# Kernel optimization log

Measured on AMD Instinct MI355X. Metric: run time of the kernel, lower is better.

The kernel has to match this reference:

```python
import jax, jax.numpy as jnp
import numpy as np

B, T, E = 2, 2048, 1024
H = 16
DH = E // H  # 64
DFF = 4 * E
EPS = 1e-5


def _layernorm(x, gamma, beta):
    mu = jnp.mean(x, axis=-1, keepdims=True)
    var = jnp.mean((x - mu) ** 2, axis=-1, keepdims=True)
    return (x - mu) * jax.lax.rsqrt(var + EPS) * gamma + beta


def setup_inputs() -> dict:
    key = jax.random.key(0)
    ks = jax.random.split(key, 16)
    s_e = 1.0 / np.sqrt(E)
    s_f = 1.0 / np.sqrt(DFF)
    return {
        "x": jax.random.normal(ks[0], (B, T, E), jnp.float32),
        # per-head QKV projections, stacked over heads [H, E, DH]
        "Wq": jax.random.normal(ks[1], (H, E, DH), jnp.float32) * s_e,
        "bq": jnp.zeros((H, DH), jnp.float32),
        "Wk": jax.random.normal(ks[2], (H, E, DH), jnp.float32) * s_e,
        "bk": jnp.zeros((H, DH), jnp.float32),
        "Wv": jax.random.normal(ks[3], (H, E, DH), jnp.float32) * s_e,
        "bv": jnp.zeros((H, DH), jnp.float32),
        # output projection
        "Wo": jax.random.normal(ks[4], (E, E), jnp.float32) * s_e,
        "bo": jnp.zeros((E,), jnp.float32),
        # feed-forward
        "W1": jax.random.normal(ks[5], (E, DFF), jnp.float32) * s_e,
        "b1": jnp.zeros((DFF,), jnp.float32),
        "W2": jax.random.normal(ks[6], (DFF, E), jnp.float32) * s_f,
        "b2": jnp.zeros((E,), jnp.float32),
        # layernorms
        "gamma1": jnp.ones((E,), jnp.float32),
        "beta1": jnp.zeros((E,), jnp.float32),
        "gamma2": jnp.ones((E,), jnp.float32),
        "beta2": jnp.zeros((E,), jnp.float32),
    }


def reference(x, Wq, bq, Wk, bk, Wv, bv, Wo, bo, W1, b1, W2, b2,
              gamma1, beta1, gamma2, beta2):
    Bc, Tc, Ec = x.shape
    # --- multi-head causal self-attention (dropout = eval/identity) ---
    xn = _layernorm(x, gamma1, beta1)
    q = jnp.einsum('bte,hed->bhtd', xn, Wq) + bq[:, None, :]
    k = jnp.einsum('bte,hed->bhtd', xn, Wk) + bk[:, None, :]
    v = jnp.einsum('bte,hed->bhtd', xn, Wv) + bv[:, None, :]
    scale = 1.0 / np.sqrt(q.shape[-1])
    scores = jnp.einsum('bhtd,bhsd->bhts', q, k) * scale  # [B,H,T,T]
    causal = jnp.tril(jnp.ones((Tc, Tc), bool))
    scores = jnp.where(causal, scores, jnp.float32(-1e9))
    attn = jax.nn.softmax(scores, axis=-1)
    out = jnp.einsum('bhts,bhsd->bhtd', attn, v)          # [B,H,T,DH]
    out = out.transpose(0, 2, 1, 3).reshape(Bc, Tc, Ec)    # concat heads
    out = out @ Wo + bo
    x = x + out
    # --- feed-forward ---
    xn2 = _layernorm(x, gamma2, beta2)
    h = jax.nn.relu(xn2 @ W1 + b1)
    x = x + (h @ W2 + b2)
    return x
```

## Files before the change

### kernel.cpp

```cpp
#include <hip/hip_runtime.h>
#include <stdint.h>

#define BT    4096
#define EDIM  1024
#define TLEN  2048
#define NH    16
#define DHH   64
#define DFFN  4096

typedef short short8 __attribute__((ext_vector_type(8)));
typedef float f32x4  __attribute__((ext_vector_type(4)));

typedef const __attribute__((address_space(1))) unsigned int* gas_ptr;
typedef __attribute__((address_space(3))) unsigned int*       las_ptr;

__device__ __forceinline__ float bf2f(unsigned short u) {
    union { unsigned int i; float f; } c; c.i = ((unsigned int)u) << 16; return c.f;
}
__device__ __forceinline__ unsigned short f2bf(float f) {
    union { float f; unsigned int i; } c; c.f = f;
    unsigned int u = c.i;
    unsigned int r = u + 0x7fffu + ((u >> 16) & 1u);
    return (unsigned short)(r >> 16);
}
__device__ __forceinline__ unsigned short f2bf_trunc(float f) {
    union { float f; unsigned int i; } c; c.f = f;
    return (unsigned short)(c.i >> 16);
}
__device__ __forceinline__ float fexp2(float x) {
#if __has_builtin(__builtin_amdgcn_exp2f)
    return __builtin_amdgcn_exp2f(x);
#else
    return __expf(x * 0.69314718056f);
#endif
}
__device__ __forceinline__ void gload16(const unsigned short* g, unsigned short* l) {
    __builtin_amdgcn_global_load_lds((gas_ptr)g, (las_ptr)l, 16, 0, 0);
}

#define CS_SCALE 0.18033688011f

template<int QKV>
__global__ __launch_bounds__(256) void transpose_kernel(
    const float* src, unsigned short* dst, int Kdim, int srcStride)
{
    __shared__ float T[64][65];
    int t = threadIdx.x;
    int n0 = blockIdx.x * 64, k0 = blockIdx.y * 64;
    int r = t >> 4, c4 = (t & 15) * 4;
    #pragma unroll
    for (int i = 0; i < 4; i++) {
        int rr = r + i * 16;
        const float* p;
        if (QKV) p = src + ((size_t)(n0 >> 6)) * 65536 + (size_t)(k0 + rr) * 64 + c4;
        else     p = src + (size_t)(k0 + rr) * srcStride + n0 + c4;
        float4 v = *(const float4*)p;
        T[c4 + 0][rr] = v.x;
        T[c4 + 1][rr] = v.y;
        T[c4 + 2][rr] = v.z;
        T[c4 + 3][rr] = v.w;
    }
    __syncthreads();
    int rn = t >> 2, ck = (t & 3) * 16;
    short8 o0, o1;
    #pragma unroll
    for (int j = 0; j < 8; j++) o0[j] = (short)f2bf(T[rn][ck + j]);
    #pragma unroll
    for (int j = 0; j < 8; j++) o1[j] = (short)f2bf(T[rn][ck + 8 + j]);
    unsigned short* dp = dst + (size_t)(n0 + rn) * Kdim + k0 + ck;
    *(short8*)dp       = o0;
    *(short8*)(dp + 8) = o1;
}

__global__ __launch_bounds__(256) void transpose_qkv3_kernel(
    const float* __restrict__ Wq, const float* __restrict__ Wk,
    const float* __restrict__ Wv, unsigned short* __restrict__ dstbase)
{
    __shared__ float T[64][65];
    int z = blockIdx.z;
    const float* src = (z == 0) ? Wq : (z == 1) ? Wk : Wv;
    unsigned short* dst = dstbase + (size_t)z * 1048576;
    int t = threadIdx.x;
    int n0 = blockIdx.x * 64, k0 = blockIdx.y * 64;
    int r = t >> 4, c4 = (t & 15) * 4;
    #pragma unroll
    for (int i = 0; i < 4; i++) {
        int rr = r + i * 16;
        const float* p = src + ((size_t)(n0 >> 6)) * 65536 + (size_t)(k0 + rr) * 64 + c4;
        float4 v = *(const float4*)p;
        T[c4 + 0][rr] = v.x;
        T[c4 + 1][rr] = v.y;
        T[c4 + 2][rr] = v.z;
        T[c4 + 3][rr] = v.w;
    }
    __syncthreads();
    int rn = t >> 2, ck = (t & 3) * 16;
    short8 o0, o1;
    #pragma unroll
    for (int j = 0; j < 8; j++) o0[j] = (short)f2bf(T[rn][ck + j]);
    #pragma unroll
    for (int j = 0; j < 8; j++) o1[j] = (short)f2bf(T[rn][ck + 8 + j]);
    unsigned short* dp = dst + (size_t)(n0 + rn) * EDIM + k0 + ck;
    *(short8*)dp       = o0;
    *(short8*)(dp + 8) = o1;
}

__global__ __launch_bounds__(256) void transpose_ffn_kernel(
    const float* __restrict__ W1h, const float* __restrict__ W2h,
    unsigned short* __restrict__ w1t, unsigned short* __restrict__ w2t)
{
    __shared__ float T[64][65];
    int z = blockIdx.z;
    const float* src;
    unsigned short* dst;
    int Kdim, sstride, n0, k0;
    if (z == 0) { src = W1h; dst = w1t; Kdim = 1024; sstride = 4096;
                  n0 = blockIdx.x * 64; k0 = blockIdx.y * 64; }
    else        { src = W2h; dst = w2t; Kdim = 2048; sstride = 1024;
                  n0 = blockIdx.y * 64; k0 = blockIdx.x * 64; }
    int t = threadIdx.x;
    int r = t >> 4, c4 = (t & 15) * 4;
    #pragma unroll
    for (int i = 0; i < 4; i++) {
        int rr = r + i * 16;
        const float* p = src + (size_t)(k0 + rr) * sstride + n0 + c4;
        float4 v = *(const float4*)p;
        T[c4 + 0][rr] = v.x;
        T[c4 + 1][rr] = v.y;
        T[c4 + 2][rr] = v.z;
        T[c4 + 3][rr] = v.w;
    }
    __syncthreads();
    int rn = t >> 2, ck = (t & 3) * 16;
    short8 o0, o1;
    #pragma unroll
    for (int j = 0; j < 8; j++) o0[j] = (short)f2bf(T[rn][ck + j]);
    #pragma unroll
    for (int j = 0; j < 8; j++) o1[j] = (short)f2bf(T[rn][ck + 8 + j]);
    unsigned short* dp = dst + (size_t)(n0 + rn) * Kdim + k0 + ck;
    *(short8*)dp       = o0;
    *(short8*)(dp + 8) = o1;
}

__global__ __launch_bounds__(256) void vtrans_kernel(
    const unsigned short* __restrict__ v, unsigned short* __restrict__ vt)
{
    __shared__ __align__(16) unsigned short T[64][72];
    int bh = blockIdx.x, st = blockIdx.y;
    int t = threadIdx.x;
    int r = t >> 2, c = (t & 3) * 16;
    const unsigned short* src = v + ((size_t)bh * TLEN + st * 64) * DHH;
    short8 a0 = *(const short8*)(src + r * DHH + c);
    short8 a1 = *(const short8*)(src + r * DHH + c + 8);
    *(short8*)&T[r][c]     = a0;
    *(short8*)&T[r][c + 8] = a1;
    __syncthreads();
    int d = t >> 2;
    short8 o0, o1;
    #pragma unroll
    for (int j = 0; j < 8; j++) o0[j] = (short)T[c + j][d];
    #pragma unroll
    for (int j = 0; j < 8; j++) o1[j] = (short)T[c + 8 + j][d];
    unsigned short* dst = vt + ((size_t)bh * DHH + d) * TLEN + st * 64 + c;
    *(short8*)dst       = o0;
    *(short8*)(dst + 8) = o1;
}

__global__ __launch_bounds__(256) void bias_fuse_kernel(
    const float* __restrict__ bq, const float* __restrict__ bk,
    const float* __restrict__ bv, float* __restrict__ dst)
{
    int t = blockIdx.x * 256 + threadIdx.x;
    const float* src = (t < 1024) ? bq : (t < 2048) ? bk : bv;
    dst[t] = src[t & 1023];
}

template<int F32IN>
__global__ __launch_bounds__(256) void ln_fused_kernel(
    const void* __restrict__ x, const float* __restrict__ g,
    const float* __restrict__ b, unsigned short* __restrict__ out)
{
    int row = blockIdx.x, tid = threadIdx.x;
    size_t off = (size_t)row * EDIM + tid * 4;
    float v0, v1, v2, v3;
    if (F32IN) {
        float4 a = *(const float4*)((const float*)x + off);
        v0 = a.x; v1 = a.y; v2 = a.z; v3 = a.w;
    } else {
        ushort4 raw = *(const ushort4*)((const unsigned short*)x + off);
        v0 = bf2f(raw.x); v1 = bf2f(raw.y); v2 = bf2f(raw.z); v3 = bf2f(raw.w);
    }
    float s  = v0 + v1 + v2 + v3;
    float ss = v0*v0 + v1*v1 + v2*v2 + v3*v3;
    #pragma unroll
    for (int o = 1; o < 64; o <<= 1) {
        s  += __shfl_xor(s,  o, 64);
        ss += __shfl_xor(ss, o, 64);
    }
    __shared__ float red[8];
    int wave = tid >> 6;
    if ((tid & 63) == 0) { red[wave*2] = s; red[wave*2+1] = ss; }
    __syncthreads();
    s  = red[0] + red[2] + red[4] + red[6];
    ss = red[1] + red[3] + red[5] + red[7];
    float m  = s * (1.0f / EDIM);
    float rs = rsqrtf(ss * (1.0f / EDIM) - m * m + 1e-5f);
    float4 gv = *(const float4*)(g + tid * 4);
    float4 bv = *(const float4*)(b + tid * 4);
    ushort4 o;
    o.x = f2bf((v0 - m) * rs * gv.x + bv.x);
    o.y = f2bf((v1 - m) * rs * gv.y + bv.y);
    o.z = f2bf((v2 - m) * rs * gv.z + bv.z);
    o.w = f2bf((v3 - m) * rs * gv.w + bv.w);
    *(ushort4*)(out + off) = o;
}

#define V_QKV  0
#define V_WO   1
#define V_FF1  2
#define V_FF2A 3
#define V_FF2B 4

template<int VARIANT, int BN>
__global__ __launch_bounds__(256) void gemm_bt64_kernel(
    const unsigned short* A,
    const unsigned short* Bt,
    const float* bias,
    const void* resid,
    void* out,
    int N, int K)
{
    constexpr int NJ = BN / 32;
    __shared__ __align__(16) unsigned short As[64 * 64];
    __shared__ __align__(16) unsigned short Bs[BN * 64];
    int tid  = threadIdx.x;
    int lane = tid & 63, wave = tid >> 6;
    int quad = lane >> 4, l16 = lane & 15;
    int wr = wave >> 1, wc = wave & 1;
    int m0 = blockIdx.y * 64, n0 = blockIdx.x * BN;

    f32x4 acc[2][NJ];
    #pragma unroll
    for (int i = 0; i < 2; i++)
        #pragma unroll
        for (int j = 0; j < NJ; j++) acc[i][j] = (f32x4){0.f, 0.f, 0.f, 0.f};

    int lr = lane >> 3;
    int lc = (lane & 7) * 8;

    for (int k0 = 0; k0 < K; k0 += 64) {
        #pragma unroll
        for (int i = 0; i < 2; i++) {
            int blk = i * 4 + wave;
            gload16(A + (size_t)(m0 + blk * 8 + lr) * K + k0 + lc, &As[blk * 512]);
        }
        #pragma unroll
        for (int i = 0; i < NJ; i++) {
            int blk = i * 4 + wave;
            gload16(Bt + (size_t)(n0 + blk * 8 + lr) * K + k0 + lc, &Bs[blk * 512]);
        }
        __syncthreads();

        #pragma unroll
        for (int ks = 0; ks < 2; ks++) {
            short8 af[2], bf[NJ];
            #pragma unroll
            for (int i = 0; i < 2; i++)
                af[i] = *(const short8*)(&As[(wr * 32 + i * 16 + l16) * 64 + ks * 32 + quad * 8]);
            #pragma unroll
            for (int j = 0; j < NJ; j++)
                bf[j] = *(const short8*)(&Bs[(wc * (BN / 2) + j * 16 + l16) * 64 + ks * 32 + quad * 8]);
            #pragma unroll
            for (int i = 0; i < 2; i++)
                #pragma unroll
                for (int j = 0; j < NJ; j++)
                    acc[i][j] = __builtin_amdgcn_mfma_f32_16x16x32_bf16(af[i], bf[j], acc[i][j], 0, 0, 0);
        }

        __syncthreads();
    }

    #pragma unroll
    for (int j = 0; j < NJ; j++) {
        int c = n0 + wc * (BN / 2) + j * 16 + l16;
        float bi = (VARIANT == V_FF2A) ? 0.0f : bias[c];
        #pragma unroll
        for (int i = 0; i < 2; i++) {
            #pragma unroll
            for (int r = 0; r < 4; r++) {
                int m = m0 + wr * 32 + i * 16 + quad * 4 + r;
                float val = acc[i][j][r] + bi;
                if (VARIANT == V_QKV) {
                    int b = m >> 11, t = m & 2047;
                    int mat = c >> 10, cc = c & 1023;
                    int h = cc >> 6, d = cc & 63;
                    if (mat == 0) val *= CS_SCALE;
                    ((unsigned short*)out)[(size_t)mat * 4194304 +
                        (((size_t)(b * NH + h)) * TLEN + t) * DHH + d] = f2bf(val);
                } else if (VARIANT == V_FF1) {
                    val = fmaxf(val, 0.0f);
                    ((unsigned short*)out)[(size_t)m * N + c] = f2bf(val);
                } else if (VARIANT == V_WO) {
                    val += ((const float*)resid)[(size_t)m * N + c];
                    ((unsigned short*)out)[(size_t)m * N + c] = f2bf(val);
                } else if (VARIANT == V_FF2A) {
                    ((float*)out)[(size_t)m * N + c] = val;
                } else {
                    val += bf2f(((const unsigned short*)resid)[(size_t)m * N + c])
                         + ((const float*)out)[(size_t)m * N + c];
                    ((float*)out)[(size_t)m * N + c] = val;
                }
            }
        }
    }
}

__global__ __launch_bounds__(256) void attn_kernel(
    const unsigned short* __restrict__ q,
    const unsigned short* __restrict__ k,
    const unsigned short* __restrict__ vt,
    unsigned short* __restrict__ att)
{
    __shared__ __align__(16) unsigned short Ks[128 * 72];
    __shared__ __align__(16) unsigned short Vs[64 * 136];
    __shared__ __align__(16) unsigned short Ps[4][16 * 136];
    int tid  = threadIdx.x;
    int lane = tid & 63, wave = tid >> 6;
    int quad = lane >> 4, l16 = lane & 15;

    int flat = blockIdx.x;
    int xcd  = flat & 7, idx = flat >> 3;
    int bh   = xcd * 4 + (idx >> 4);
    int pp   = idx & 15;

    const unsigned short* Kb = k  + (size_t)bh * TLEN * DHH;
    const unsigned short* Vb = vt + (size_t)bh * DHH * TLEN;
    unsigned short* Pw = Ps[wave];

    int rowK = tid >> 1, colK = (tid & 1) * 32;
    int rowV = tid >> 2, colV = (tid & 3) * 32;
    int bidx = bh >> 4, hh = bh & 15;

    for (int half = 0; half < 2; ++half) {
        int qt = half ? (31 - pp) : pp;
        int q0 = qt * 64;
        int qw = q0 + wave * 16;

        const unsigned short* Qb = q + ((size_t)bh * TLEN + qw) * DHH;
        short8 aq0 = *(const short8*)(Qb + l16 * DHH + quad * 8);
        short8 aq1 = *(const short8*)(Qb + l16 * DHH + 32 + quad * 8);

        f32x4 o[4];
        #pragma unroll
        for (int n = 0; n < 4; n++) o[n] = (f32x4){0.f, 0.f, 0.f, 0.f};
        f32x4 mrow = {-1e30f, -1e30f, -1e30f, -1e30f};
        f32x4 lrow = {0.f, 0.f, 0.f, 0.f};

        int nch = (q0 >> 7) + 1;

        short8 ka0, ka1, ka2, ka3, va0, va1, va2, va3;
        {
            const unsigned short* kp = Kb + (size_t)rowK * DHH + colK;
            ka0 = *(const short8*)kp;
            ka1 = *(const short8*)(kp + 8);
            ka2 = *(const short8*)(kp + 16);
            ka3 = *(const short8*)(kp + 24);
            const unsigned short* vp = Vb + (size_t)rowV * TLEN + colV;
            va0 = *(const short8*)vp;
            va1 = *(const short8*)(vp + 8);
            va2 = *(const short8*)(vp + 16);
            va3 = *(const short8*)(vp + 24);
        }

        for (int ch = 0; ch < nch; ch++) {
            int s0 = ch * 128;
            __syncthreads();
            *(short8*)(&Ks[rowK * 72 + colK])       = ka0;
            *(short8*)(&Ks[rowK * 72 + colK + 8])   = ka1;
            *(short8*)(&Ks[rowK * 72 + colK + 16])  = ka2;
            *(short8*)(&Ks[rowK * 72 + colK + 24])  = ka3;
            *(short8*)(&Vs[rowV * 136 + colV])      = va0;
            *(short8*)(&Vs[rowV * 136 + colV + 8])  = va1;
            *(short8*)(&Vs[rowV * 136 + colV + 16]) = va2;
            *(short8*)(&Vs[rowV * 136 + colV + 24]) = va3;
            __syncthreads();

            if (ch + 1 < nch) {
                int s1 = s0 + 128;
                const unsigned short* kp = Kb + (size_t)(s1 + rowK) * DHH + colK;
                ka0 = *(const short8*)kp;
                ka1 = *(const short8*)(kp + 8);
                ka2 = *(const short8*)(kp + 16);
                ka3 = *(const short8*)(kp + 24);
                const unsigned short* vp = Vb + (size_t)rowV * TLEN + s1 + colV;
                va0 = *(const short8*)vp;
                va1 = *(const short8*)(vp + 8);
                va2 = *(const short8*)(vp + 16);
                va3 = *(const short8*)(vp + 24);
            }

            f32x4 S[8];
            #pragma unroll
            for (int n = 0; n < 8; n++) {
                short8 b0 = *(const short8*)(&Ks[(n * 16 + l16) * 72 + quad * 8]);
                short8 b1 = *(const short8*)(&Ks[(n * 16 + l16) * 72 + 32 + quad * 8]);
                f32x4 s = (f32x4){0.f, 0.f, 0.f, 0.f};
                s = __builtin_amdgcn_mfma_f32_16x16x32_bf16(aq0, b0, s, 0, 0, 0);
                s = __builtin_amdgcn_mfma_f32_16x16x32_bf16(aq1, b1, s, 0, 0, 0);
                S[n] = s;
            }
            bool needmask = (s0 + 127 > qw);
            #pragma unroll
            for (int r = 0; r < 4; r++) {
                float xv[8];
                #pragma unroll
                for (int n = 0; n < 8; n++) {
                    float xx = S[n][r];
                    if (needmask && (s0 + n * 16 + l16 > qw + quad * 4 + r)) xx = -1e30f;
                    xv[n] = xx;
                }
                float mxl = fmaxf(fmaxf(fmaxf(xv[0], xv[1]), fmaxf(xv[2], xv[3])),
                                  fmaxf(fmaxf(xv[4], xv[5]), fmaxf(xv[6], xv[7])));
                float used;
                if (__all(mxl <= mrow[r] + 8.0f)) {
                    used = mrow[r];
                } else {
                    float mx = mxl;
                    mx = fmaxf(mx, __shfl_xor(mx, 1, 64));
                    mx = fmaxf(mx, __shfl_xor(mx, 2, 64));
                    mx = fmaxf(mx, __shfl_xor(mx, 4, 64));
                    mx = fmaxf(mx, __shfl_xor(mx, 8, 64));
                    float mnew  = fmaxf(mrow[r], mx);
                    float alpha = fexp2(mrow[r] - mnew);
                    lrow[r] *= alpha;
                    o[0][r] *= alpha; o[1][r] *= alpha;
                    o[2][r] *= alpha; o[3][r] *= alpha;
                    mrow[r] = mnew;
                    used = mnew;
                }
                float ps = 0.f;
                int prow = (quad * 4 + r) * 136;
                #pragma unroll
                for (int n = 0; n < 8; n++) {
                    float p = fexp2(xv[n] - used);
                    ps += p;
                    Pw[prow + n * 16 + l16] = f2bf_trunc(p);
                }
                lrow[r] += ps;
            }
            short8 ap[4];
            #pragma unroll
            for (int ks = 0; ks < 4; ks++)
                ap[ks] = *(const short8*)(Pw + l16 * 136 + ks * 32 + quad * 8);
            #pragma unroll
            for (int n = 0; n < 4; n++) {
                #pragma unroll
                for (int ks = 0; ks < 4; ks++) {
                    short8 b = *(const short8*)(&Vs[(n * 16 + l16) * 136 + ks * 32 + quad * 8]);
                    o[n] = __builtin_amdgcn_mfma_f32_16x16x32_bf16(ap[ks], b, o[n], 0, 0, 0);
                }
            }
        }

        #pragma unroll
        for (int r = 0; r < 4; r++) {
            float ls = lrow[r];
            ls += __shfl_xor(ls, 1, 64);
            ls += __shfl_xor(ls, 2, 64);
            ls += __shfl_xor(ls, 4, 64);
            ls += __shfl_xor(ls, 8, 64);
            float inv = 1.0f / ls;
            int t = qw + quad * 4 + r;
            size_t rowoff = ((size_t)(bidx * TLEN + t)) * EDIM + hh * 64;
            #pragma unroll
            for (int n = 0; n < 4; n++)
                att[rowoff + n * 16 + l16] = f2bf(o[n][r] * inv);
        }
    }
}

extern "C" void kernel_launch(void* const* d_in, const int* in_sizes, int n_in,
                              void* d_out, int out_size, void* d_ws, size_t ws_size,
                              hipStream_t stream)
{
    (void)in_sizes; (void)n_in; (void)out_size; (void)ws_size;
    const float* x   = (const float*)d_in[0];
    const float* Wq  = (const float*)d_in[1];
    const float* bq  = (const float*)d_in[2];
    const float* Wk  = (const float*)d_in[3];
    const float* bk  = (const float*)d_in[4];
    const float* Wv  = (const float*)d_in[5];
    const float* bv  = (const float*)d_in[6];
    const float* Wo  = (const float*)d_in[7];
    const float* bo  = (const float*)d_in[8];
    const float* W1  = (const float*)d_in[9];
    const float* b1  = (const float*)d_in[10];
    const float* W2  = (const float*)d_in[11];
    const float* b2  = (const float*)d_in[12];
    const float* g1  = (const float*)d_in[13];
    const float* be1 = (const float*)d_in[14];
    const float* g2  = (const float*)d_in[15];
    const float* be2 = (const float*)d_in[16];

    unsigned short* ws  = (unsigned short*)d_ws;
    unsigned short* xn  = ws;
    unsigned short* vtg = ws;
    unsigned short* qb  = ws + 4194304;
    unsigned short* kb  = ws + 8388608;
    unsigned short* vb  = ws + 12582912;
    unsigned short* wqt = ws + 16777216;
    unsigned short* att = ws + 16777216;
    unsigned short* x1  = ws + 4194304;
    unsigned short* wot = ws + 8388608;
    unsigned short* w1t = ws + 8388608;
    unsigned short* w2t = ws + 10485760;
    unsigned short* hb  = ws + 12582912;
    float* biasf = (float*)(ws + 19922944);

    dim3 gT64(16, 16);
    dim3 gE64(EDIM / 64, BT / 64);
    dim3 gQKV(3072 / 128, BT / 64);
    dim3 gF(2048 / 128, BT / 64);

    transpose_qkv3_kernel<<<dim3(16, 16, 3), 256, 0, stream>>>(Wq, Wk, Wv, wqt);
    bias_fuse_kernel<<<dim3(12), 256, 0, stream>>>(bq, bk, bv, biasf);

    ln_fused_kernel<1><<<BT, 256, 0, stream>>>(x, g1, be1, xn);

    gemm_bt64_kernel<V_QKV, 128><<<gQKV, 256, 0, stream>>>(xn, wqt, biasf, nullptr, qb, 3072, EDIM);

    vtrans_kernel<<<dim3(NH * 2, TLEN / 64), 256, 0, stream>>>(vb, vtg);

    attn_kernel<<<dim3(512), 256, 0, stream>>>(qb, kb, vtg, att);

    transpose_kernel<0><<<gT64, 256, 0, stream>>>(Wo, wot, EDIM, EDIM);
    gemm_bt64_kernel<V_WO, 64><<<gE64, 256, 0, stream>>>(att, wot, bo, x, x1, EDIM, EDIM);

    ln_fused_kernel<0><<<BT, 256, 0, stream>>>(x1, g2, be2, xn);

    transpose_ffn_kernel<<<dim3(32, 16, 2), 256, 0, stream>>>(W1, W2, w1t, w2t);
    gemm_bt64_kernel<V_FF1, 128><<<gF, 256, 0, stream>>>(xn, w1t, b1, nullptr, hb, 2048, EDIM);
    gemm_bt64_kernel<V_FF2A, 64><<<gE64, 256, 0, stream>>>(hb, w2t, nullptr, nullptr, d_out, EDIM, 2048);
    transpose_ffn_kernel<<<dim3(32, 16, 2), 256, 0, stream>>>(W1 + 2048, W2 + (size_t)2048 * EDIM, w1t, w2t);
    gemm_bt64_kernel<V_FF1, 128><<<gF, 256, 0, stream>>>(xn, w1t, b1 + 2048, nullptr, hb, 2048, EDIM);
    gemm_bt64_kernel<V_FF2B, 64><<<gE64, 256, 0, stream>>>(hb, w2t, b2, x1, d_out, EDIM, 2048);
}
```

Baseline: 408.5 us.

## Transpose QK^T MFMA so each lane owns one query row; drop bias fuse kernel

The attention score MFMA now has its operands swapped, so the score tile comes out transposed and each lane holds one query row across four key columns. Online softmax max and sum then need only two cross-lane shuffles per chunk instead of per-row reductions over 16 lanes. P is written to LDS as packed bf16 pairs, and the rescale and normalise factors are broadcast to the output rows with shuffles. Separately, the QKV GEMM reads bq, bk and bv directly, which removes the bias_fuse launch at the cost of a per-column select in the epilogue.

```diff
diff --git a/kernel.cpp b/kernel.cpp
--- a/kernel.cpp
+++ b/kernel.cpp
@@ -23,16 +23,16 @@
     unsigned int r = u + 0x7fffu + ((u >> 16) & 1u);
     return (unsigned short)(r >> 16);
 }
-__device__ __forceinline__ unsigned short f2bf_trunc(float f) {
-    union { float f; unsigned int i; } c; c.f = f;
-    return (unsigned short)(c.i >> 16);
-}
 __device__ __forceinline__ float fexp2(float x) {
 #if __has_builtin(__builtin_amdgcn_exp2f)
     return __builtin_amdgcn_exp2f(x);
 #else
     return __expf(x * 0.69314718056f);
 #endif
+}
+__device__ __forceinline__ unsigned int pack_bf2(float a, float b) {
+    union { float f; unsigned int i; } ca, cb; ca.f = a; cb.f = b;
+    return (cb.i & 0xFFFF0000u) | (ca.i >> 16);
 }
 __device__ __forceinline__ void gload16(const unsigned short* g, unsigned short* l) {
     __builtin_amdgcn_global_load_lds((gas_ptr)g, (las_ptr)l, 16, 0, 0);
@@ -164,15 +164,6 @@
     unsigned short* dst = vt + ((size_t)bh * DHH + d) * TLEN + st * 64 + c;
     *(short8*)dst       = o0;
     *(short8*)(dst + 8) = o1;
-}
-
-__global__ __launch_bounds__(256) void bias_fuse_kernel(
-    const float* __restrict__ bq, const float* __restrict__ bk,
-    const float* __restrict__ bv, float* __restrict__ dst)
-{
-    int t = blockIdx.x * 256 + threadIdx.x;
-    const float* src = (t < 1024) ? bq : (t < 2048) ? bk : bv;
-    dst[t] = src[t & 1023];
 }
 
 template<int F32IN>
@@ -226,6 +217,8 @@
     const unsigned short* A,
     const unsigned short* Bt,
     const float* bias,
+    const float* bias2,
+    const float* bias3,
     const void* resid,
     void* out,
     int N, int K)
@@ -283,7 +276,13 @@
     #pragma unroll
     for (int j = 0; j < NJ; j++) {
         int c = n0 + wc * (BN / 2) + j * 16 + l16;
-        float bi = (VARIANT == V_FF2A) ? 0.0f : bias[c];
+        float bi;
+        if (VARIANT == V_QKV) {
+            int mat = c >> 10, cc = c & 1023;
+            bi = (mat == 0 ? bias : mat == 1 ? bias2 : bias3)[cc];
+        } else {
+            bi = (VARIANT == V_FF2A) ? 0.0f : bias[c];
+        }
         #pragma unroll
         for (int i = 0; i < 2; i++) {
             #pragma unroll
@@ -345,6 +344,7 @@
         int qt = half ? (31 - pp) : pp;
         int q0 = qt * 64;
         int qw = q0 + wave * 16;
+        int qme = qw + l16;
 
         const unsigned short* Qb = q + ((size_t)bh * TLEN + qw) * DHH;
         short8 aq0 = *(const short8*)(Qb + l16 * DHH + quad * 8);
@@ -353,8 +353,8 @@
         f32x4 o[4];
         #pragma unroll
         for (int n = 0; n < 4; n++) o[n] = (f32x4){0.f, 0.f, 0.f, 0.f};
-        f32x4 mrow = {-1e30f, -1e30f, -1e30f, -1e30f};
-        f32x4 lrow = {0.f, 0.f, 0.f, 0.f};
+        float mreg = -1e30f;
+        float lreg = 0.f;
 
         int nch = (q0 >> 7) + 1;
 
@@ -405,48 +405,52 @@
                 short8 b0 = *(const short8*)(&Ks[(n * 16 + l16) * 72 + quad * 8]);
                 short8 b1 = *(const short8*)(&Ks[(n * 16 + l16) * 72 + 32 + quad * 8]);
                 f32x4 s = (f32x4){0.f, 0.f, 0.f, 0.f};
-                s = __builtin_amdgcn_mfma_f32_16x16x32_bf16(aq0, b0, s, 0, 0, 0);
-                s = __builtin_amdgcn_mfma_f32_16x16x32_bf16(aq1, b1, s, 0, 0, 0);
+                s = __builtin_amdgcn_mfma_f32_16x16x32_bf16(b0, aq0, s, 0, 0, 0);
+                s = __builtin_amdgcn_mfma_f32_16x16x32_bf16(b1, aq1, s, 0, 0, 0);
                 S[n] = s;
             }
             bool needmask = (s0 + 127 > qw);
-            #pragma unroll
-            for (int r = 0; r < 4; r++) {
-                float xv[8];
+
+            float mxl = -1e30f;
+            #pragma unroll
+            for (int n = 0; n < 8; n++) {
                 #pragma unroll
-                for (int n = 0; n < 8; n++) {
+                for (int r = 0; r < 4; r++) {
                     float xx = S[n][r];
-                    if (needmask && (s0 + n * 16 + l16 > qw + quad * 4 + r)) xx = -1e30f;
-                    xv[n] = xx;
+                    if (needmask && (s0 + n * 16 + quad * 4 + r > qme)) xx = -1e30f;
+                    S[n][r] = xx;
+                    mxl = fmaxf(mxl, xx);
                 }
-                float mxl = fmaxf(fmaxf(fmaxf(xv[0], xv[1]), fmaxf(xv[2], xv[3])),
-                                  fmaxf(fmaxf(xv[4], xv[5]), fmaxf(xv[6], xv[7])));
-                float used;
-                if (__all(mxl <= mrow[r] + 8.0f)) {
-                    used = mrow[r];
-                } else {
-                    float mx = mxl;
-                    mx = fmaxf(mx, __shfl_xor(mx, 1, 64));
-                    mx = fmaxf(mx, __shfl_xor(mx, 2, 64));
-                    mx = fmaxf(mx, __shfl_xor(mx, 4, 64));
-                    mx = fmaxf(mx, __shfl_xor(mx, 8, 64));
-                    float mnew  = fmaxf(mrow[r], mx);
-                    float alpha = fexp2(mrow[r] - mnew);
-                    lrow[r] *= alpha;
-                    o[0][r] *= alpha; o[1][r] *= alpha;
-                    o[2][r] *= alpha; o[3][r] *= alpha;
-                    mrow[r] = mnew;
-                    used = mnew;
+            }
+            float used;
+            if (__all(mxl <= mreg + 8.0f)) {
+                used = mreg;
+            } else {
+                float mx = mxl;
+                mx = fmaxf(mx, __shfl_xor(mx, 16, 64));
+                mx = fmaxf(mx, __shfl_xor(mx, 32, 64));
+                float mnew  = fmaxf(mreg, mx);
+                float alpha = fexp2(mreg - mnew);
+                lreg *= alpha;
+                #pragma unroll
+                for (int r = 0; r < 4; r++) {
+                    float ar = __shfl(alpha, quad * 4 + r, 16);
+                    o[0][r] *= ar; o[1][r] *= ar;
+                    o[2][r] *= ar; o[3][r] *= ar;
                 }
-                float ps = 0.f;
-                int prow = (quad * 4 + r) * 136;
-                #pragma unroll
-                for (int n = 0; n < 8; n++) {
-                    float p = fexp2(xv[n] - used);
-                    ps += p;
-                    Pw[prow + n * 16 + l16] = f2bf_trunc(p);
-                }
-                lrow[r] += ps;
+                mreg = mnew;
+                used = mnew;
+            }
+            #pragma unroll
+            for (int n = 0; n < 8; n++) {
+                float p0 = fexp2(S[n][0] - used);
+                float p1 = fexp2(S[n][1] - used);
+                float p2 = fexp2(S[n][2] - used);
+                float p3 = fexp2(S[n][3] - used);
+                lreg += (p0 + p1) + (p2 + p3);
+                int sp = l16 * 136 + n * 16 + quad * 4;
+                *(unsigned int*)(Pw + sp)     = pack_bf2(p0, p1);
+                *(unsigned int*)(Pw + sp + 2) = pack_bf2(p2, p3);
             }
             short8 ap[4];
             #pragma unroll
@@ -462,19 +466,18 @@
             }
         }
 
+        float ls = lreg;
+        ls += __shfl_xor(ls, 16, 64);
+        ls += __shfl_xor(ls, 32, 64);
+        float inv = 1.0f / ls;
         #pragma unroll
         for (int r = 0; r < 4; r++) {
-            float ls = lrow[r];
-            ls += __shfl_xor(ls, 1, 64);
-            ls += __shfl_xor(ls, 2, 64);
-            ls += __shfl_xor(ls, 4, 64);
-            ls += __shfl_xor(ls, 8, 64);
-            float inv = 1.0f / ls;
+            float invr = __shfl(inv, quad * 4 + r, 16);
             int t = qw + quad * 4 + r;
             size_t rowoff = ((size_t)(bidx * TLEN + t)) * EDIM + hh * 64;
             #pragma unroll
             for (int n = 0; n < 4; n++)
-                att[rowoff + n * 16 + l16] = f2bf(o[n][r] * inv);
+                att[rowoff + n * 16 + l16] = f2bf(o[n][r] * invr);
         }
     }
 }
@@ -515,7 +518,6 @@
     unsigned short* w1t = ws + 8388608;
     unsigned short* w2t = ws + 10485760;
     unsigned short* hb  = ws + 12582912;
-    float* biasf = (float*)(ws + 19922944);
 
     dim3 gT64(16, 16);
     dim3 gE64(EDIM / 64, BT / 64);
@@ -523,25 +525,24 @@
     dim3 gF(2048 / 128, BT / 64);
 
     transpose_qkv3_kernel<<<dim3(16, 16, 3), 256, 0, stream>>>(Wq, Wk, Wv, wqt);
-    bias_fuse_kernel<<<dim3(12), 256, 0, stream>>>(bq, bk, bv, biasf);
 
     ln_fused_kernel<1><<<BT, 256, 0, stream>>>(x, g1, be1, xn);
 
-    gemm_bt64_kernel<V_QKV, 128><<<gQKV, 256, 0, stream>>>(xn, wqt, biasf, nullptr, qb, 3072, EDIM);
+    gemm_bt64_kernel<V_QKV, 128><<<gQKV, 256, 0, stream>>>(xn, wqt, bq, bk, bv, nullptr, qb, 3072, EDIM);
 
     vtrans_kernel<<<dim3(NH * 2, TLEN / 64), 256, 0, stream>>>(vb, vtg);
 
     attn_kernel<<<dim3(512), 256, 0, stream>>>(qb, kb, vtg, att);
 
     transpose_kernel<0><<<gT64, 256, 0, stream>>>(Wo, wot, EDIM, EDIM);
-    gemm_bt64_kernel<V_WO, 64><<<gE64, 256, 0, stream>>>(att, wot, bo, x, x1, EDIM, EDIM);
+    gemm_bt64_kernel<V_WO, 64><<<gE64, 256, 0, stream>>>(att, wot, bo, nullptr, nullptr, x, x1, EDIM, EDIM);
 
     ln_fused_kernel<0><<<BT, 256, 0, stream>>>(x1, g2, be2, xn);
 
     transpose_ffn_kernel<<<dim3(32, 16, 2), 256, 0, stream>>>(W1, W2, w1t, w2t);
-    gemm_bt64_kernel<V_FF1, 128><<<gF, 256, 0, stream>>>(xn, w1t, b1, nullptr, hb, 2048, EDIM);
-    gemm_bt64_kernel<V_FF2A, 64><<<gE64, 256, 0, stream>>>(hb, w2t, nullptr, nullptr, d_out, EDIM, 2048);
+    gemm_bt64_kernel<V_FF1, 128><<<gF, 256, 0, stream>>>(xn, w1t, b1, nullptr, nullptr, nullptr, hb, 2048, EDIM);
+    gemm_bt64_kernel<V_FF2A, 64><<<gE64, 256, 0, stream>>>(hb, w2t, nullptr, nullptr, nullptr, nullptr, d_out, EDIM, 2048);
     transpose_ffn_kernel<<<dim3(32, 16, 2), 256, 0, stream>>>(W1 + 2048, W2 + (size_t)2048 * EDIM, w1t, w2t);
-    gemm_bt64_kernel<V_FF1, 128><<<gF, 256, 0, stream>>>(xn, w1t, b1 + 2048, nullptr, hb, 2048, EDIM);
-    gemm_bt64_kernel<V_FF2B, 64><<<gE64, 256, 0, stream>>>(hb, w2t, b2, x1, d_out, EDIM, 2048);
-}
+    gemm_bt64_kernel<V_FF1, 128><<<gF, 256, 0, stream>>>(xn, w1t, b1 + 2048, nullptr, nullptr, nullptr, hb, 2048, EDIM);
+    gemm_bt64_kernel<V_FF2B, 64><<<gE64, 256, 0, stream>>>(hb, w2t, b2, nullptr, nullptr, x1, d_out, EDIM, 2048);
+}
```

After: 398.4 us. 2.5% less time.
